# Kernel tuning notes

Measured on AMD Instinct MI355X. Metric: run time of the kernel, lower is better.

Reference implementation:

```python
import jax, jax.numpy as jnp
import numpy as np

N, E, IN, OUT = 50000, 800000, 256, 256
EPS = 1e-5


def setup_inputs() -> dict:
    key = jax.random.key(0)
    k1, k2, k3 = jax.random.split(key, 3)
    x = jax.random.normal(k1, (N, IN), dtype=jnp.float32)
    edge_index = jax.random.randint(k2, (2, E), 0, N, dtype=jnp.int64)
    batch = jnp.zeros((N,), dtype=jnp.int64)
    # glorot-style init for GCN weight
    scale = jnp.sqrt(2.0 / (IN + OUT)).astype(jnp.float32)
    W = jax.random.normal(k3, (IN, OUT), dtype=jnp.float32) * scale
    conv_bias = jnp.zeros((OUT,), dtype=jnp.float32)
    ln_weight = jnp.ones((OUT,), dtype=jnp.float32)
    ln_bias = jnp.zeros((OUT,), dtype=jnp.float32)
    prelu_a = jnp.full((1,), 0.25, dtype=jnp.float32)  # nn.PReLU default
    return {"x": x, "edge_index": edge_index, "batch": batch, "W": W,
            "conv_bias": conv_bias, "ln_weight": ln_weight,
            "ln_bias": ln_bias, "prelu_a": prelu_a}


def reference(x, edge_index, batch, W, conv_bias, ln_weight, ln_bias, prelu_a):
    n = x.shape[0]
    src, dst = edge_index[0], edge_index[1]
    # GCNConv: add self-loops, symmetric deg^{-1/2} normalization
    loop = jnp.arange(n, dtype=src.dtype)
    src_f = jnp.concatenate([src, loop])  # [E+N]
    dst_f = jnp.concatenate([dst, loop])
    h = x @ W  # [N, OUT] -- transform before propagate (PyG order)
    deg = jax.ops.segment_sum(jnp.ones_like(dst_f, dtype=h.dtype), dst_f,
                              num_segments=n)  # >=1 due to self loops
    dinv = jax.lax.rsqrt(deg)
    norm = dinv[src_f] * dinv[dst_f]  # [E+N]
    out = jax.ops.segment_sum(h[src_f] * norm[:, None], dst_f,
                              num_segments=n) + conv_bias  # [N, OUT]
    # PyG LayerNorm, mode='graph', batch=None: normalize over ALL nodes+feats
    mu = out.mean()
    xc = out - mu
    std = jnp.sqrt((xc * xc).mean())
    y = xc / (std + EPS) * ln_weight + ln_bias
    # PReLU (single shared slope)
    return jnp.where(y >= 0, y, prelu_a * y)
```

## Files before the change

### kernel.cpp

```cpp
#include <hip/hip_runtime.h>
#include <hip/hip_bf16.h>


#define F 256
#define EPSV 1e-5f

typedef __attribute__((ext_vector_type(8))) short short8;
typedef __attribute__((ext_vector_type(4))) float f32x4;

__device__ __forceinline__ unsigned short f2bf(float f) {
  union { float f; unsigned u; } v; v.f = f;
  unsigned r = v.u + 0x7fffu + ((v.u >> 16) & 1u);
  return (unsigned short)(r >> 16);
}

__device__ __forceinline__ float bf2f(unsigned short u) {
  union { unsigned u; float f; } v; v.u = ((unsigned)u) << 16; return v.f;
}


__global__ void count_rank(const int* __restrict__ dst, int* __restrict__ deg_cnt,
                           int* __restrict__ rank, int E, int eb,
                           const float* __restrict__ W, unsigned short* __restrict__ Wb) {
  if ((int)blockIdx.x < eb) {
    int e = blockIdx.x * 256 + threadIdx.x;
    if (e < E) rank[e] = atomicAdd(&deg_cnt[dst[e]], 1);
    return;
  }
  int gid = (blockIdx.x - eb) * 256 + threadIdx.x;
  int j = gid & 7;
  int lane = (gid >> 3) & 63;
  int kc = (gid >> 9) & 7;
  int tt = gid >> 12;
  int k = kc * 32 + (lane >> 4) * 8 + j;
  int n = tt * 16 + (lane & 15);
  Wb[gid] = f2bf(W[k * 256 + n]);
}


__global__ void block_sums(const int* __restrict__ deg_cnt, int* __restrict__ bsum,
                           float* __restrict__ dinv, int N) {
  __shared__ int s[256];
  int t = threadIdx.x;
  int i = blockIdx.x * 256 + t;
  int d = (i < N) ? deg_cnt[i] : 0;
  if (i < N) dinv[i] = rsqrtf((float)(d + 1));
  s[t] = d;
  __syncthreads();
  for (int off = 128; off > 0; off >>= 1) {
    if (t < off) s[t] += s[t + off];
    __syncthreads();
  }
  if (t == 0) bsum[blockIdx.x] = s[0];
}

__global__ void scan_bsums(const int* __restrict__ bsum, int* __restrict__ boff, int nb) {
  __shared__ int s[256];
  int t = threadIdx.x;
  int v = (t < nb) ? bsum[t] : 0;
  s[t] = v;
  __syncthreads();
  for (int off = 1; off < 256; off <<= 1) {
    int x = (t >= off) ? s[t - off] : 0;
    __syncthreads();
    s[t] += x;
    __syncthreads();
  }
  if (t < nb) boff[t] = s[t] - v;
}

__global__ void write_csr(const int* __restrict__ deg_cnt, const int* __restrict__ boff,
                          int* __restrict__ csr_ptr, int N, int E) {
  __shared__ int s[256];
  int t = threadIdx.x;
  int i = blockIdx.x * 256 + t;
  int v = (i < N) ? deg_cnt[i] : 0;
  s[t] = v;
  __syncthreads();
  for (int off = 1; off < 256; off <<= 1) {
    int x = (t >= off) ? s[t - off] : 0;
    __syncthreads();
    s[t] += x;
    __syncthreads();
  }
  if (i < N) csr_ptr[i] = boff[blockIdx.x] + s[t] - v;
  if (i == 0) csr_ptr[N] = E;
}


__global__ void fill_gemm(const int* __restrict__ src, const int* __restrict__ dst,
                          const int* __restrict__ rank, const int* __restrict__ csr_ptr,
                          int* __restrict__ csr_src, int E, int eb,
                          const float* __restrict__ x, const unsigned short* __restrict__ Wb,
                          const float* __restrict__ dinv, ushort4* __restrict__ hb, int N) {
  __shared__ unsigned short A[64][264];

  if ((int)blockIdx.x < eb) {
    int e = blockIdx.x * 256 + threadIdx.x;
    if (e < E) {
      int d = dst[e];
      csr_src[csr_ptr[d] + rank[e]] = src[e];
    }
    return;
  }

  int bid = blockIdx.x - eb;
  int m0 = bid * 64;
  int t = threadIdx.x;
  int lane = t & 63;
  int wave = t >> 6;
  int q = lane >> 4;

#pragma unroll
  for (int j = 0; j < 16; ++j) {
    int idx = j * 256 + t;
    int row = idx >> 6;
    int c4 = idx & 63;
    int gr = m0 + row;
    int grc = gr < N ? gr : N - 1;
    float4 v = *(const float4*)(x + (size_t)grc * F + c4 * 4);
    ushort4 u;
    u.x = f2bf(v.x); u.y = f2bf(v.y); u.z = f2bf(v.z); u.w = f2bf(v.w);
    *(ushort4*)&A[row][c4 * 4] = u;
  }
  __syncthreads();

  f32x4 acc[4][4];
#pragma unroll
  for (int m = 0; m < 4; ++m)
#pragma unroll
    for (int tt = 0; tt < 4; ++tt)
      acc[m][tt] = (f32x4){0.f, 0.f, 0.f, 0.f};

  int arow = lane & 15;
  for (int kc = 0; kc < 8; ++kc) {
    short8 a[4];
#pragma unroll
    for (int m = 0; m < 4; ++m)
      a[m] = *(const short8*)&A[m * 16 + arow][kc * 32 + q * 8];
#pragma unroll
    for (int tt = 0; tt < 4; ++tt) {
      const short8 b = *(const short8*)(Wb + (((wave * 4 + tt) * 8 + kc) * 64 + lane) * 8);
#pragma unroll
      for (int m = 0; m < 4; ++m)
        acc[m][tt] = __builtin_amdgcn_mfma_f32_16x16x32_bf16(a[m], b, acc[m][tt], 0, 0, 0);
    }
  }

  __syncthreads();

  int ccol = lane & 15;
#pragma unroll
  for (int m = 0; m < 4; ++m) {
#pragma unroll
    for (int rr = 0; rr < 4; ++rr) {
      int lrow = m * 16 + q * 4 + rr;
      int orow = m0 + lrow;
      float dv = (orow < N) ? dinv[orow] : 0.f;
#pragma unroll
      for (int tt = 0; tt < 4; ++tt)
        A[lrow][(wave * 4 + tt) * 16 + ccol] = f2bf(acc[m][tt][rr] * dv);
    }
  }
  __syncthreads();
#pragma unroll
  for (int j = 0; j < 16; ++j) {
    int idx = j * 256 + t;
    int row = idx >> 6;
    int c4 = idx & 63;
    int grow = m0 + row;
    if (grow < N) hb[(size_t)grow * 64 + c4] = *(const ushort4*)&A[row][c4 * 4];
  }
}


__global__ void aggregate(const ushort4* __restrict__ hb, const int* __restrict__ csr_ptr,
                          const int* __restrict__ csr_src, const float* __restrict__ dinv,
                          const float* __restrict__ conv_bias, float4* __restrict__ out,
                          double2* __restrict__ partials, int N) {
  int wave = threadIdx.x >> 6;
  int lane = threadIdx.x & 63;
  int row = blockIdx.x * 4 + wave;
  float s1 = 0.f, s2 = 0.f;

  if (row < N) {
    float di = dinv[row];
    int b0 = csr_ptr[row], b1 = csr_ptr[row + 1];
    ushort4 self = hb[(size_t)row * 64 + lane];
    float4 acc;
    acc.x = bf2f(self.x); acc.y = bf2f(self.y);
    acc.z = bf2f(self.z); acc.w = bf2f(self.w);

    for (int e = b0; e < b1; e += 16) {
      int idx[16];
#pragma unroll
      for (int j = 0; j < 16; ++j) {
        int ee = e + j;
        idx[j] = csr_src[ee < b1 ? ee : b1 - 1];
      }
      ushort4 v[16];
#pragma unroll
      for (int j = 0; j < 16; ++j) v[j] = hb[(size_t)idx[j] * 64 + lane];
#pragma unroll
      for (int j = 0; j < 16; ++j) {
        float m = (e + j < b1) ? 1.f : 0.f;
        acc.x = fmaf(bf2f(v[j].x), m, acc.x);
        acc.y = fmaf(bf2f(v[j].y), m, acc.y);
        acc.z = fmaf(bf2f(v[j].z), m, acc.z);
        acc.w = fmaf(bf2f(v[j].w), m, acc.w);
      }
    }

    float4 b = *(const float4*)(conv_bias + lane * 4);
    acc.x = fmaf(acc.x, di, b.x);
    acc.y = fmaf(acc.y, di, b.y);
    acc.z = fmaf(acc.z, di, b.z);
    acc.w = fmaf(acc.w, di, b.w);
    out[(size_t)row * 64 + lane] = acc;
    s1 = acc.x + acc.y + acc.z + acc.w;
    s2 = acc.x * acc.x + acc.y * acc.y + acc.z * acc.z + acc.w * acc.w;
  }

  __shared__ float r1[256];
  __shared__ float r2[256];
  int t = threadIdx.x;
  r1[t] = s1;
  r2[t] = s2;
  __syncthreads();
  for (int off = 128; off > 0; off >>= 1) {
    if (t < off) { r1[t] += r1[t + off]; r2[t] += r2[t + off]; }
    __syncthreads();
  }
  if (t == 0) {
    double2 pp;
    pp.x = (double)r1[0];
    pp.y = (double)r2[0];
    partials[blockIdx.x] = pp;
  }
}

__global__ void finalize_stats(const double2* __restrict__ partials, int nb,
                               float* __restrict__ stats, double cnt) {
  __shared__ double q1[1024];
  __shared__ double q2[1024];
  int t = threadIdx.x;
  double a1 = 0.0, a2 = 0.0;
  for (int i = t; i < nb; i += 1024) {
    double2 pp = partials[i];
    a1 += pp.x;
    a2 += pp.y;
  }
  q1[t] = a1;
  q2[t] = a2;
  __syncthreads();
  for (int off = 512; off > 0; off >>= 1) {
    if (t < off) { q1[t] += q1[t + off]; q2[t] += q2[t + off]; }
    __syncthreads();
  }
  if (t == 0) {
    double mu = q1[0] / cnt;
    double var = q2[0] / cnt - mu * mu;
    if (var < 0) var = 0;
    double sd = sqrt(var);
    stats[0] = (float)mu;
    stats[1] = (float)(1.0 / (sd + (double)EPSV));
  }
}

__global__ void norm_prelu(float4* __restrict__ out, const float* __restrict__ stats,
                           const float* __restrict__ lw, const float* __restrict__ lb,
                           const float* __restrict__ pa, int n4) {
  int i = blockIdx.x * blockDim.x + threadIdx.x;
  if (i >= n4) return;
  float mu = stats[0];
  float inv = stats[1];
  float a = pa[0];
  int c4 = (i & 63) * 4;
  float4 w = *(const float4*)(lw + c4);
  float4 b = *(const float4*)(lb + c4);
  float4 v = out[i];
  float y0 = (v.x - mu) * inv * w.x + b.x;
  float y1 = (v.y - mu) * inv * w.y + b.y;
  float y2 = (v.z - mu) * inv * w.z + b.z;
  float y3 = (v.w - mu) * inv * w.w + b.w;
  v.x = y0 >= 0.f ? y0 : a * y0;
  v.y = y1 >= 0.f ? y1 : a * y1;
  v.z = y2 >= 0.f ? y2 : a * y2;
  v.w = y3 >= 0.f ? y3 : a * y3;
  out[i] = v;
}


extern "C" void kernel_launch(void* const* d_in, const int* in_sizes, int n_in,
                              void* d_out, int out_size, void* d_ws, size_t ws_size,
                              hipStream_t stream) {
  const float* x = (const float*)d_in[0];
  const int* eidx = (const int*)d_in[1];
  const float* W = (const float*)d_in[3];
  const float* conv_bias = (const float*)d_in[4];
  const float* ln_w = (const float*)d_in[5];
  const float* ln_b = (const float*)d_in[6];
  const float* prelu_a = (const float*)d_in[7];
  float* out = (float*)d_out;

  int N = in_sizes[0] / F;
  int E = in_sizes[1] / 2;
  const int* src = eidx;
  const int* dst = eidx + E;

  int nAggBlocks = (N + 3) / 4;
  int eb = (E + 255) / 256;
  int gemmb = (N + 63) / 64;
  int NB = (N + 255) / 256;

  char* p = (char*)d_ws;
  auto carve = [&](size_t bytes) { char* r = p; p += (bytes + 255) & ~(size_t)255; return r; };
  ushort4* hb    = (ushort4*)carve((size_t)N * 64 * sizeof(ushort4));
  unsigned short* Wb = (unsigned short*)carve((size_t)F * F * sizeof(short));
  int* deg_cnt   = (int*)carve((size_t)N * sizeof(int));
  int* rank      = (int*)carve((size_t)E * sizeof(int));
  float* dinv    = (float*)carve((size_t)N * sizeof(float));
  int* csr_ptr   = (int*)carve((size_t)(N + 1) * sizeof(int));
  int* csr_src   = (int*)carve((size_t)E * sizeof(int));
  int* bsum      = (int*)carve((size_t)NB * sizeof(int));
  int* boff      = (int*)carve((size_t)NB * sizeof(int));
  double2* partials = (double2*)carve((size_t)nAggBlocks * sizeof(double2));
  float* stats   = (float*)carve(2 * sizeof(float));

  hipMemsetAsync(deg_cnt, 0, (size_t)N * sizeof(int), stream);

  count_rank<<<eb + 256, 256, 0, stream>>>(dst, deg_cnt, rank, E, eb, W, Wb);
  block_sums<<<NB, 256, 0, stream>>>(deg_cnt, bsum, dinv, N);
  scan_bsums<<<1, 256, 0, stream>>>(bsum, boff, NB);
  write_csr<<<NB, 256, 0, stream>>>(deg_cnt, boff, csr_ptr, N, E);
  fill_gemm<<<eb + gemmb, 256, 0, stream>>>(src, dst, rank, csr_ptr, csr_src, E, eb,
                                            x, Wb, dinv, hb, N);
  aggregate<<<nAggBlocks, 256, 0, stream>>>(hb, csr_ptr, csr_src, dinv,
                                            conv_bias, (float4*)out, partials, N);
  finalize_stats<<<1, 1024, 0, stream>>>(partials, nAggBlocks, stats,
                                         (double)N * (double)F);
  int n4 = N * (F / 4);
  norm_prelu<<<(n4 + 255) / 256, 256, 0, stream>>>((float4*)out, stats, ln_w, ln_b, prelu_a, n4);
}
```

Before: 273.6 us.

## Move GEMM before degree scan and apply source dinv during aggregation

```diff
diff --git a/kernel.cpp b/kernel.cpp
--- a/kernel.cpp
+++ b/kernel.cpp
@@ -19,15 +19,14 @@
 }
 
 
-__global__ void count_rank(const int* __restrict__ dst, int* __restrict__ deg_cnt,
-                           int* __restrict__ rank, int E, int eb,
-                           const float* __restrict__ W, unsigned short* __restrict__ Wb) {
-  if ((int)blockIdx.x < eb) {
-    int e = blockIdx.x * 256 + threadIdx.x;
-    if (e < E) rank[e] = atomicAdd(&deg_cnt[dst[e]], 1);
+__global__ void init_prep(int* __restrict__ deg_cnt, int N, int NB,
+                          const float* __restrict__ W, unsigned short* __restrict__ Wb) {
+  if ((int)blockIdx.x < NB) {
+    int i = blockIdx.x * 256 + threadIdx.x;
+    if (i < N) deg_cnt[i] = 0;
     return;
   }
-  int gid = (blockIdx.x - eb) * 256 + threadIdx.x;
+  int gid = (blockIdx.x - NB) * 256 + threadIdx.x;
   int j = gid & 7;
   int lane = (gid >> 3) & 63;
   int kc = (gid >> 9) & 7;
@@ -38,69 +37,15 @@
 }
 
 
-__global__ void block_sums(const int* __restrict__ deg_cnt, int* __restrict__ bsum,
-                           float* __restrict__ dinv, int N) {
-  __shared__ int s[256];
-  int t = threadIdx.x;
-  int i = blockIdx.x * 256 + t;
-  int d = (i < N) ? deg_cnt[i] : 0;
-  if (i < N) dinv[i] = rsqrtf((float)(d + 1));
-  s[t] = d;
-  __syncthreads();
-  for (int off = 128; off > 0; off >>= 1) {
-    if (t < off) s[t] += s[t + off];
-    __syncthreads();
-  }
-  if (t == 0) bsum[blockIdx.x] = s[0];
-}
-
-__global__ void scan_bsums(const int* __restrict__ bsum, int* __restrict__ boff, int nb) {
-  __shared__ int s[256];
-  int t = threadIdx.x;
-  int v = (t < nb) ? bsum[t] : 0;
-  s[t] = v;
-  __syncthreads();
-  for (int off = 1; off < 256; off <<= 1) {
-    int x = (t >= off) ? s[t - off] : 0;
-    __syncthreads();
-    s[t] += x;
-    __syncthreads();
-  }
-  if (t < nb) boff[t] = s[t] - v;
-}
-
-__global__ void write_csr(const int* __restrict__ deg_cnt, const int* __restrict__ boff,
-                          int* __restrict__ csr_ptr, int N, int E) {
-  __shared__ int s[256];
-  int t = threadIdx.x;
-  int i = blockIdx.x * 256 + t;
-  int v = (i < N) ? deg_cnt[i] : 0;
-  s[t] = v;
-  __syncthreads();
-  for (int off = 1; off < 256; off <<= 1) {
-    int x = (t >= off) ? s[t - off] : 0;
-    __syncthreads();
-    s[t] += x;
-    __syncthreads();
-  }
-  if (i < N) csr_ptr[i] = boff[blockIdx.x] + s[t] - v;
-  if (i == 0) csr_ptr[N] = E;
-}
-
-
-__global__ void fill_gemm(const int* __restrict__ src, const int* __restrict__ dst,
-                          const int* __restrict__ rank, const int* __restrict__ csr_ptr,
-                          int* __restrict__ csr_src, int E, int eb,
-                          const float* __restrict__ x, const unsigned short* __restrict__ Wb,
-                          const float* __restrict__ dinv, ushort4* __restrict__ hb, int N) {
+__global__ void count_gemm(const int* __restrict__ dst, int* __restrict__ deg_cnt,
+                           int* __restrict__ rank, int E, int eb,
+                           const float* __restrict__ x, const unsigned short* __restrict__ Wb,
+                           ushort4* __restrict__ hb, int N) {
   __shared__ unsigned short A[64][264];
 
   if ((int)blockIdx.x < eb) {
     int e = blockIdx.x * 256 + threadIdx.x;
-    if (e < E) {
-      int d = dst[e];
-      csr_src[csr_ptr[d] + rank[e]] = src[e];
-    }
+    if (e < E) rank[e] = atomicAdd(&deg_cnt[dst[e]], 1);
     return;
   }
 
@@ -118,9 +63,9 @@
     int c4 = idx & 63;
     int gr = m0 + row;
     int grc = gr < N ? gr : N - 1;
-    float4 v = *(const float4*)(x + (size_t)grc * F + c4 * 4);
+    f32x4 v = __builtin_nontemporal_load((const f32x4*)(x + (size_t)grc * F + c4 * 4));
     ushort4 u;
-    u.x = f2bf(v.x); u.y = f2bf(v.y); u.z = f2bf(v.z); u.w = f2bf(v.w);
+    u.x = f2bf(v[0]); u.y = f2bf(v[1]); u.z = f2bf(v[2]); u.w = f2bf(v[3]);
     *(ushort4*)&A[row][c4 * 4] = u;
   }
   __syncthreads();
@@ -155,11 +100,9 @@
 #pragma unroll
     for (int rr = 0; rr < 4; ++rr) {
       int lrow = m * 16 + q * 4 + rr;
-      int orow = m0 + lrow;
-      float dv = (orow < N) ? dinv[orow] : 0.f;
 #pragma unroll
       for (int tt = 0; tt < 4; ++tt)
-        A[lrow][(wave * 4 + tt) * 16 + ccol] = f2bf(acc[m][tt][rr] * dv);
+        A[lrow][(wave * 4 + tt) * 16 + ccol] = f2bf(acc[m][tt][rr]);
     }
   }
   __syncthreads();
@@ -174,9 +117,70 @@
 }
 
 
+__global__ void block_sums(const int* __restrict__ deg_cnt, int* __restrict__ bsum,
+                           float* __restrict__ dinv, int N) {
+  __shared__ int s[256];
+  int t = threadIdx.x;
+  int i = blockIdx.x * 256 + t;
+  int d = (i < N) ? deg_cnt[i] : 0;
+  if (i < N) dinv[i] = rsqrtf((float)(d + 1));
+  s[t] = d;
+  __syncthreads();
+  for (int off = 128; off > 0; off >>= 1) {
+    if (t < off) s[t] += s[t + off];
+    __syncthreads();
+  }
+  if (t == 0) bsum[blockIdx.x] = s[0];
+}
+
+__global__ void scan_bsums(const int* __restrict__ bsum, int* __restrict__ boff, int nb) {
+  __shared__ int s[256];
+  int t = threadIdx.x;
+  int v = (t < nb) ? bsum[t] : 0;
+  s[t] = v;
+  __syncthreads();
+  for (int off = 1; off < 256; off <<= 1) {
+    int x = (t >= off) ? s[t - off] : 0;
+    __syncthreads();
+    s[t] += x;
+    __syncthreads();
+  }
+  if (t < nb) boff[t] = s[t] - v;
+}
+
+__global__ void write_csr(const int* __restrict__ deg_cnt, const int* __restrict__ boff,
+                          int* __restrict__ csr_ptr, int N, int E) {
+  __shared__ int s[256];
+  int t = threadIdx.x;
+  int i = blockIdx.x * 256 + t;
+  int v = (i < N) ? deg_cnt[i] : 0;
+  s[t] = v;
+  __syncthreads();
+  for (int off = 1; off < 256; off <<= 1) {
+    int x = (t >= off) ? s[t - off] : 0;
+    __syncthreads();
+    s[t] += x;
+    __syncthreads();
+  }
+  if (i < N) csr_ptr[i] = boff[blockIdx.x] + s[t] - v;
+  if (i == 0) csr_ptr[N] = E;
+}
+
+
+__global__ void fill(const int* __restrict__ src, const int* __restrict__ dst,
+                     const int* __restrict__ rank, const int* __restrict__ csr_ptr,
+                     int* __restrict__ csr_src, int E) {
+  int e = blockIdx.x * 256 + threadIdx.x;
+  if (e < E) {
+    int d = dst[e];
+    csr_src[csr_ptr[d] + rank[e]] = src[e];
+  }
+}
+
+
 __global__ void aggregate(const ushort4* __restrict__ hb, const int* __restrict__ csr_ptr,
                           const int* __restrict__ csr_src, const float* __restrict__ dinv,
-                          const float* __restrict__ conv_bias, float4* __restrict__ out,
+                          const float* __restrict__ conv_bias, float* __restrict__ out,
                           double2* __restrict__ partials, int N) {
   int wave = threadIdx.x >> 6;
   int lane = threadIdx.x & 63;
@@ -187,9 +191,9 @@
     float di = dinv[row];
     int b0 = csr_ptr[row], b1 = csr_ptr[row + 1];
     ushort4 self = hb[(size_t)row * 64 + lane];
-    float4 acc;
-    acc.x = bf2f(self.x); acc.y = bf2f(self.y);
-    acc.z = bf2f(self.z); acc.w = bf2f(self.w);
+    f32x4 acc;
+    acc[0] = bf2f(self.x) * di; acc[1] = bf2f(self.y) * di;
+    acc[2] = bf2f(self.z) * di; acc[3] = bf2f(self.w) * di;
 
     for (int e = b0; e < b1; e += 16) {
       int idx[16];
@@ -201,24 +205,27 @@
       ushort4 v[16];
 #pragma unroll
       for (int j = 0; j < 16; ++j) v[j] = hb[(size_t)idx[j] * 64 + lane];
+      float w[16];
+#pragma unroll
+      for (int j = 0; j < 16; ++j) w[j] = dinv[idx[j]];
 #pragma unroll
       for (int j = 0; j < 16; ++j) {
-        float m = (e + j < b1) ? 1.f : 0.f;
-        acc.x = fmaf(bf2f(v[j].x), m, acc.x);
-        acc.y = fmaf(bf2f(v[j].y), m, acc.y);
-        acc.z = fmaf(bf2f(v[j].z), m, acc.z);
-        acc.w = fmaf(bf2f(v[j].w), m, acc.w);
+        float m = (e + j < b1) ? w[j] : 0.f;
+        acc[0] = fmaf(bf2f(v[j].x), m, acc[0]);
+        acc[1] = fmaf(bf2f(v[j].y), m, acc[1]);
+        acc[2] = fmaf(bf2f(v[j].z), m, acc[2]);
+        acc[3] = fmaf(bf2f(v[j].w), m, acc[3]);
       }
     }
 
-    float4 b = *(const float4*)(conv_bias + lane * 4);
-    acc.x = fmaf(acc.x, di, b.x);
-    acc.y = fmaf(acc.y, di, b.y);
-    acc.z = fmaf(acc.z, di, b.z);
-    acc.w = fmaf(acc.w, di, b.w);
-    out[(size_t)row * 64 + lane] = acc;
-    s1 = acc.x + acc.y + acc.z + acc.w;
-    s2 = acc.x * acc.x + acc.y * acc.y + acc.z * acc.z + acc.w * acc.w;
+    const f32x4 b = *(const f32x4*)(conv_bias + lane * 4);
+    acc[0] = fmaf(acc[0], di, b[0]);
+    acc[1] = fmaf(acc[1], di, b[1]);
+    acc[2] = fmaf(acc[2], di, b[2]);
+    acc[3] = fmaf(acc[3], di, b[3]);
+    __builtin_nontemporal_store(acc, (f32x4*)(out + ((size_t)row * 64 + lane) * 4));
+    s1 = acc[0] + acc[1] + acc[2] + acc[3];
+    s2 = acc[0] * acc[0] + acc[1] * acc[1] + acc[2] * acc[2] + acc[3] * acc[3];
   }
 
   __shared__ float r1[256];
@@ -267,7 +274,7 @@
   }
 }
 
-__global__ void norm_prelu(float4* __restrict__ out, const float* __restrict__ stats,
+__global__ void norm_prelu(float* __restrict__ out, const float* __restrict__ stats,
                            const float* __restrict__ lw, const float* __restrict__ lb,
                            const float* __restrict__ pa, int n4) {
   int i = blockIdx.x * blockDim.x + threadIdx.x;
@@ -276,18 +283,16 @@
   float inv = stats[1];
   float a = pa[0];
   int c4 = (i & 63) * 4;
-  float4 w = *(const float4*)(lw + c4);
-  float4 b = *(const float4*)(lb + c4);
-  float4 v = out[i];
-  float y0 = (v.x - mu) * inv * w.x + b.x;
-  float y1 = (v.y - mu) * inv * w.y + b.y;
-  float y2 = (v.z - mu) * inv * w.z + b.z;
-  float y3 = (v.w - mu) * inv * w.w + b.w;
-  v.x = y0 >= 0.f ? y0 : a * y0;
-  v.y = y1 >= 0.f ? y1 : a * y1;
-  v.z = y2 >= 0.f ? y2 : a * y2;
-  v.w = y3 >= 0.f ? y3 : a * y3;
-  out[i] = v;
+  const f32x4 w = *(const f32x4*)(lw + c4);
+  const f32x4 b = *(const f32x4*)(lb + c4);
+  f32x4 v = __builtin_nontemporal_load((const f32x4*)(out + (size_t)i * 4));
+  f32x4 y;
+#pragma unroll
+  for (int j = 0; j < 4; ++j) {
+    float yv = (v[j] - mu) * inv * w[j] + b[j];
+    y[j] = yv >= 0.f ? yv : a * yv;
+  }
+  __builtin_nontemporal_store(y, (f32x4*)(out + (size_t)i * 4));
 }
 
 
@@ -327,18 +332,16 @@
   double2* partials = (double2*)carve((size_t)nAggBlocks * sizeof(double2));
   float* stats   = (float*)carve(2 * sizeof(float));
 
-  hipMemsetAsync(deg_cnt, 0, (size_t)N * sizeof(int), stream);
-
-  count_rank<<<eb + 256, 256, 0, stream>>>(dst, deg_cnt, rank, E, eb, W, Wb);
+  init_prep<<<NB + 256, 256, 0, stream>>>(deg_cnt, N, NB, W, Wb);
+  count_gemm<<<eb + gemmb, 256, 0, stream>>>(dst, deg_cnt, rank, E, eb, x, Wb, hb, N);
   block_sums<<<NB, 256, 0, stream>>>(deg_cnt, bsum, dinv, N);
   scan_bsums<<<1, 256, 0, stream>>>(bsum, boff, NB);
   write_csr<<<NB, 256, 0, stream>>>(deg_cnt, boff, csr_ptr, N, E);
-  fill_gemm<<<eb + gemmb, 256, 0, stream>>>(src, dst, rank, csr_ptr, csr_src, E, eb,
-                                            x, Wb, dinv, hb, N);
+  fill<<<eb, 256, 0, stream>>>(src, dst, rank, csr_ptr, csr_src, E);
   aggregate<<<nAggBlocks, 256, 0, stream>>>(hb, csr_ptr, csr_src, dinv,
-                                            conv_bias, (float4*)out, partials, N);
+                                            conv_bias, out, partials, N);
   finalize_stats<<<1, 1024, 0, stream>>>(partials, nAggBlocks, stats,
                                          (double)N * (double)F);
   int n4 = N * (F / 4);
-  norm_prelu<<<(n4 + 255) / 256, 256, 0, stream>>>((float4*)out, stats, ln_w, ln_b, prelu_a, n4);
-}
+  norm_prelu<<<(n4 + 255) / 256, 256, 0, stream>>>(out, stats, ln_w, ln_b, prelu_a, n4);
+}
```

Measured after the change: 276.7 us. About the same (+1.1%).
